# Kernel tuning notes

Hardware: AMD Instinct MI355X
Metric: run time of the kernel (lower is better)

The kernel has to match this reference:

```python
import jax, jax.numpy as jnp
import numpy as np

B, S, D, H = 32, 512, 768, 12
HD = D // H
FF = 4 * D
EPS = 1e-5


def layernorm(x, g, b):
    mu = jnp.mean(x, axis=-1, keepdims=True)
    var = jnp.mean(jnp.square(x - mu), axis=-1, keepdims=True)
    return (x - mu) * jax.lax.rsqrt(var + EPS) * g + b


def setup_inputs() -> dict:
    key = jax.random.key(0)
    ks = jax.random.split(key, 10)
    s = 0.02
    return {
        "x": jax.random.normal(ks[0], (B, S, D), jnp.float32),
        "edge_bias": jax.random.normal(ks[1], (H, S, S), jnp.float32) * s,
        "ln1_g": jnp.ones((D,), jnp.float32),
        "ln1_b": jnp.zeros((D,), jnp.float32),
        "qkv_w": jax.random.normal(ks[2], (3 * D, D), jnp.float32) * s,
        "qkv_b": jnp.zeros((3 * D,), jnp.float32),
        "proj_w": jax.random.normal(ks[3], (D, D), jnp.float32) * s,
        "proj_b": jnp.zeros((D,), jnp.float32),
        "ln2_g": jnp.ones((D,), jnp.float32),
        "ln2_b": jnp.zeros((D,), jnp.float32),
        "fc1_w": jax.random.normal(ks[4], (FF, D), jnp.float32) * s,
        "fc1_b": jnp.zeros((FF,), jnp.float32),
        "fc2_w": jax.random.normal(ks[5], (D, FF), jnp.float32) * s,
        "fc2_b": jnp.zeros((D,), jnp.float32),
    }


def reference(x, edge_bias, ln1_g, ln1_b, qkv_w, qkv_b, proj_w, proj_b,
              ln2_g, ln2_b, fc1_w, fc1_b, fc2_w, fc2_b):
    shortcut = x
    xn = layernorm(x, ln1_g, ln1_b)
    # qkv: [B,S,3D] -> [3,B,H,S,HD]
    qkv = (xn @ qkv_w.T + qkv_b).reshape(B, S, 3, H, HD).transpose(2, 0, 3, 1, 4)
    q, k, v = qkv[0], qkv[1], qkv[2]
    q = q * (HD ** -0.5)
    attn = jnp.einsum('bhqd,bhkd->bhqk', q, k) + edge_bias[None]
    attn = jax.nn.softmax(attn, axis=-1)
    o = jnp.einsum('bhqk,bhkd->bhqd', attn, v)
    o = o.transpose(0, 2, 1, 3).reshape(B, S, D)
    o = o @ proj_w.T + proj_b
    x = shortcut + o
    h = layernorm(x, ln2_g, ln2_b)
    h = jax.nn.gelu(h @ fc1_w.T + fc1_b, approximate=False)
    h = h @ fc2_w.T + fc2_b
    return x + h
```

## Files before the change

kernel.cpp:

```cpp
#include <hip/hip_runtime.h>

typedef unsigned short u16;
typedef unsigned int u32;
typedef float f32x4 __attribute__((ext_vector_type(4)));
typedef __bf16 bf16x8 __attribute__((ext_vector_type(8)));

__device__ __forceinline__ u16 f2bf(float f) {
  u32 u = __float_as_uint(f);
  u += 0x7fffu + ((u >> 16) & 1u);
  return (u16)(u >> 16);
}

__device__ __forceinline__ float bf2f(u16 v) {
  return __uint_as_float((u32)v << 16);
}

__device__ __forceinline__ void gload16(const u16* g, u16* l) {
  __builtin_amdgcn_global_load_lds(
      (__attribute__((address_space(1))) void*)(u16*)g,
      (__attribute__((address_space(3))) void*)l, 16, 0, 0);
}

__global__ __launch_bounds__(256) void cvt_bf16(const float* __restrict__ in,
                                                u16* __restrict__ o, int n4) {
  int i = blockIdx.x * 256 + threadIdx.x;
  if (i >= n4) return;
  float4 f = reinterpret_cast<const float4*>(in)[i];
  u32 lo = (u32)f2bf(f.x) | ((u32)f2bf(f.y) << 16);
  u32 hi = (u32)f2bf(f.z) | ((u32)f2bf(f.w) << 16);
  reinterpret_cast<uint2*>(o)[i] = make_uint2(lo, hi);
}

__global__ __launch_bounds__(256) void cvt_w_pack(const float* __restrict__ in,
                                                  u16* __restrict__ o, int N, int K) {
  int i = blockIdx.x * 256 + threadIdx.x;
  const int ng = K >> 3;
  if (i >= N * ng) return;
  const int n = i / ng;
  const int k = (i - n * ng) * 8;
  const float4 f0 = reinterpret_cast<const float4*>(in + (size_t)n * K + k)[0];
  const float4 f1 = reinterpret_cast<const float4*>(in + (size_t)n * K + k)[1];
  u32 p0 = (u32)f2bf(f0.x) | ((u32)f2bf(f0.y) << 16);
  u32 p1 = (u32)f2bf(f0.z) | ((u32)f2bf(f0.w) << 16);
  u32 p2 = (u32)f2bf(f1.x) | ((u32)f2bf(f1.y) << 16);
  u32 p3 = (u32)f2bf(f1.z) | ((u32)f2bf(f1.w) << 16);
  u16* dst = o + ((size_t)(k >> 5) * N + n) * 32 + (k & 31);
  reinterpret_cast<uint4*>(dst)[0] = make_uint4(p0, p1, p2, p3);
}

__global__ __launch_bounds__(256) void ln_bf16(const float* __restrict__ x,
                                               const float* __restrict__ g,
                                               const float* __restrict__ b,
                                               u16* __restrict__ o) {
  const int row = blockIdx.x;
  const int t = threadIdx.x;
  const float* xr = x + (size_t)row * 768;
  float a0 = xr[t], a1 = xr[t + 256], a2 = xr[t + 512];
  float s = a0 + a1 + a2;
  float ss = a0 * a0 + a1 * a1 + a2 * a2;
#pragma unroll
  for (int m = 1; m < 64; m <<= 1) {
    s += __shfl_xor(s, m);
    ss += __shfl_xor(ss, m);
  }
  __shared__ float sb[8];
  if ((t & 63) == 0) { sb[t >> 6] = s; sb[4 + (t >> 6)] = ss; }
  __syncthreads();
  s = sb[0] + sb[1] + sb[2] + sb[3];
  ss = sb[4] + sb[5] + sb[6] + sb[7];
  const float mu = s * (1.0f / 768.0f);
  const float var = ss * (1.0f / 768.0f) - mu * mu;
  const float rs = rsqrtf(var + 1e-5f);
#pragma unroll
  for (int c = 0; c < 3; ++c) {
    const int col = t + c * 256;
    const float a = (c == 0) ? a0 : (c == 1) ? a1 : a2;
    o[((size_t)(col >> 5) * 16384 + row) * 32 + (col & 31)] =
        f2bf((a - mu) * rs * g[col] + b[col]);
  }
}

enum { EPI_QKV = 0, EPI_PROJ = 1, EPI_GELU = 2, EPI_OUT = 3 };

template <int EPI>
__global__ __launch_bounds__(512, 2) void gemm_bt(
    const u16* __restrict__ A, const u16* __restrict__ W,
    const float* __restrict__ bias, const float* __restrict__ res,
    float* __restrict__ outf, u16* __restrict__ outb,
    u16* __restrict__ outq, u16* __restrict__ outk, u16* __restrict__ outv,
    int M, int N, int K) {
  __shared__ u16 SA[4 * 8192];
  __shared__ u16 SB[4 * 8192];
  const int tid = threadIdx.x;
  const int wid = tid >> 6, l = tid & 63;
  const int wm = wid >> 2, wn = wid & 3;
  const int lg = l >> 4, lc = l & 15;

  const u32 nbn = gridDim.x;
  const u32 orig = blockIdx.y * nbn + blockIdx.x;
  const u32 cpx = (nbn * gridDim.y) >> 3;
  const u32 wgid = (orig & 7) * cpx + (orig >> 3);
  const int bn = wgid % nbn;
  const int bm = wgid / nbn;

  const size_t Msl = (size_t)M * 32;
  const size_t Nsl = (size_t)N * 32;
  const size_t lane_a = (size_t)(bm * 256 + wid * 16 + (l >> 2)) * 32 +
                        (((l & 3) ^ ((l >> 3) & 3)) << 3);
  const size_t lane_w = (size_t)(bn * 256 + wid * 16 + (l >> 2)) * 32 +
                        (((l & 3) ^ ((l >> 3) & 3)) << 3);

  const int sg = (lg ^ ((lc >> 1) & 3)) << 3;

  f32x4 acc[8][4] = {};

  const int NU = K >> 5;

#define STAGE(u)                                                      \
  {                                                                   \
    const int slot_ = (u) & 3;                                        \
    const u16* Au_ = A + (size_t)(u) * Msl + lane_a;                  \
    const u16* Wu_ = W + (size_t)(u) * Nsl + lane_w;                  \
    gload16(Au_, &SA[slot_ * 8192 + wid * 512]);                      \
    gload16(Au_ + 4096, &SA[slot_ * 8192 + 4096 + wid * 512]);        \
    gload16(Wu_, &SB[slot_ * 8192 + wid * 512]);                      \
    gload16(Wu_ + 4096, &SB[slot_ * 8192 + 4096 + wid * 512]);        \
  }

  STAGE(0);
  STAGE(1);
  STAGE(2);
  asm volatile("s_waitcnt vmcnt(8)" ::: "memory");
  __builtin_amdgcn_s_barrier();

  for (int u = 0; u < NU; ++u) {
    const u16* sa = &SA[(u & 3) * 8192];
    const u16* sb = &SB[(u & 3) * 8192];
    bf16x8 af[8], bf[4];
#pragma unroll
    for (int mi = 0; mi < 8; ++mi)
      af[mi] = *reinterpret_cast<const bf16x8*>(&sa[(wm * 128 + mi * 16 + lc) * 32 + sg]);
#pragma unroll
    for (int ni = 0; ni < 4; ++ni)
      bf[ni] = *reinterpret_cast<const bf16x8*>(&sb[(wn * 64 + ni * 16 + lc) * 32 + sg]);
    if (u + 3 < NU) STAGE(u + 3);
    __builtin_amdgcn_s_barrier();
    __builtin_amdgcn_s_setprio(1);
#pragma unroll
    for (int mi = 0; mi < 8; ++mi)
#pragma unroll
      for (int ni = 0; ni < 4; ++ni)
        acc[mi][ni] = __builtin_amdgcn_mfma_f32_16x16x32_bf16(af[mi], bf[ni], acc[mi][ni], 0, 0, 0);
    __builtin_amdgcn_s_setprio(0);
    if (u + 3 < NU) {
      asm volatile("s_waitcnt vmcnt(8)" ::: "memory");
    } else if (u + 2 < NU) {
      asm volatile("s_waitcnt vmcnt(4)" ::: "memory");
    } else if (u + 1 < NU) {
      asm volatile("s_waitcnt vmcnt(0)" ::: "memory");
    }
    __builtin_amdgcn_s_barrier();
  }
#undef STAGE

  const int rbase = bm * 256 + wm * 128;
  const int cbase = bn * 256 + wn * 64;
#pragma unroll
  for (int mi = 0; mi < 8; ++mi) {
#pragma unroll
    for (int ni = 0; ni < 4; ++ni) {
#pragma unroll
      for (int r = 0; r < 4; ++r) {
        const int i = rbase + mi * 16 + lg * 4 + r;
        const int j = cbase + ni * 16 + lc;
        float v = acc[mi][ni][r] + bias[j];
        if constexpr (EPI == EPI_QKV) {
          const int t = j / 768;
          const int rr = j - t * 768;
          const int h = rr >> 6, hd = rr & 63;
          const int bb = i >> 9, ssi = i & 511;
          if (t == 0) {
            outq[((size_t)(bb * 12 + h) * 512 + ssi) * 64 + hd] = f2bf(v * 0.125f);
          } else if (t == 1) {
            outk[((size_t)(bb * 12 + h) * 512 + ssi) * 64 + hd] = f2bf(v);
          } else {
            outv[((size_t)(bb * 12 + h) * 64 + hd) * 512 + ssi] = f2bf(v);
          }
        } else if constexpr (EPI == EPI_PROJ) {
          outf[(size_t)i * 768 + j] = v + res[(size_t)i * 768 + j];
        } else if constexpr (EPI == EPI_GELU) {
          float gl = 0.5f * v * (1.0f + erff(v * 0.70710678118654752f));
          outb[((size_t)(j >> 5) * 16384 + i) * 32 + (j & 31)] = f2bf(gl);
        } else {
          outf[(size_t)i * 768 + j] = v + res[(size_t)i * 768 + j];
        }
      }
    }
  }
}

__global__ __launch_bounds__(256) void attn_fwd(const u16* __restrict__ q,
                                                const u16* __restrict__ k,
                                                const u16* __restrict__ vt,
                                                const u16* __restrict__ ebb,
                                                u16* __restrict__ o) {
  __shared__ u16 Ks[128 * 64];
  __shared__ u16 Vs[64 * 128];
  __shared__ u16 Bs[64 * 128];
  __shared__ u16 P[4 * 1024];
  const int tid = threadIdx.x;
  const int w = tid >> 6, l = tid & 63;
  const int lg = l >> 4, lc = l & 15;
  const int xcd = blockIdx.x & 7;
  const int wg = xcd * 384 + (blockIdx.x >> 3);
  const int qt = wg & 7;
  const int b = (wg >> 3) & 31;
  const int h = wg >> 8;
  const int bh = b * 12 + h;
  const int q0 = qt * 64;
  const u16* qp = q + (size_t)bh * 512 * 64;
  const u16* kp = k + (size_t)bh * 512 * 64;
  const u16* vtp = vt + (size_t)bh * 64 * 512;
  const u16* ep = ebb + (size_t)h * 262144 + (size_t)q0 * 512;

  bf16x8 aq[2];
#pragma unroll
  for (int kk = 0; kk < 2; ++kk)
    aq[kk] = *reinterpret_cast<const bf16x8*>(qp + (q0 + w * 16 + lc) * 64 + kk * 32 + lg * 8);

  float m[4], lsum[4];
  f32x4 oa[4] = {};
#pragma unroll
  for (int r = 0; r < 4; ++r) { m[r] = -1e30f; lsum[r] = 0.f; }

  const int krow_l = l >> 3;
  const int kgr = ((l & 7) ^ (l >> 3)) << 3;
  const int vrow_l = l >> 4;
  const int vswz = 4 * (w & 1) + (l >> 4);
  const int vgr = (((l & 15) ^ vswz)) << 3;
  const int bgr = (l & 15) << 3;
  char* Pw = (char*)&P[w * 1024];

  for (int kc = 0; kc < 4; ++kc) {
    const int kb = kc * 128;
    __syncthreads();
#pragma unroll
    for (int i = 0; i < 4; ++i) {
      const int grp = i * 4 + w;
      gload16(kp + (size_t)(kb + grp * 8 + krow_l) * 64 + kgr, &Ks[grp * 512]);
      gload16(vtp + (size_t)(grp * 4 + vrow_l) * 512 + kb + vgr, &Vs[grp * 512]);
      gload16(ep + (size_t)(grp * 4 + vrow_l) * 512 + kb + bgr, &Bs[grp * 512]);
    }
    __syncthreads();

    f32x4 s[8] = {};
#pragma unroll
    for (int kt = 0; kt < 8; ++kt) {
      const int kbyte = (kt * 16 + lc) * 128;
      const int sw = lc & 7;
      bf16x8 b0 = *reinterpret_cast<const bf16x8*>((const char*)Ks + kbyte + ((lg ^ sw) << 4));
      bf16x8 b1 = *reinterpret_cast<const bf16x8*>((const char*)Ks + kbyte + (((4 + lg) ^ sw) << 4));
      s[kt] = __builtin_amdgcn_mfma_f32_16x16x32_bf16(aq[0], b0, s[kt], 0, 0, 0);
      s[kt] = __builtin_amdgcn_mfma_f32_16x16x32_bf16(aq[1], b1, s[kt], 0, 0, 0);
    }
#pragma unroll
    for (int kt = 0; kt < 8; ++kt)
#pragma unroll
      for (int r = 0; r < 4; ++r)
        s[kt][r] += bf2f(Bs[(w * 16 + lg * 4 + r) * 128 + kt * 16 + lc]);
#pragma unroll
    for (int r = 0; r < 4; ++r) {
      float mc = s[0][r];
#pragma unroll
      for (int kt = 1; kt < 8; ++kt) mc = fmaxf(mc, s[kt][r]);
      mc = fmaxf(mc, __shfl_xor(mc, 1));
      mc = fmaxf(mc, __shfl_xor(mc, 2));
      mc = fmaxf(mc, __shfl_xor(mc, 4));
      mc = fmaxf(mc, __shfl_xor(mc, 8));
      const float mn = fmaxf(m[r], mc);
      const float al = __expf(m[r] - mn);
      m[r] = mn;
      float sum = 0.f;
#pragma unroll
      for (int kt = 0; kt < 8; ++kt) {
        float pv = __expf(s[kt][r] - mn);
        s[kt][r] = pv;
        sum += pv;
      }
      sum += __shfl_xor(sum, 1);
      sum += __shfl_xor(sum, 2);
      sum += __shfl_xor(sum, 4);
      sum += __shfl_xor(sum, 8);
      lsum[r] = lsum[r] * al + sum;
#pragma unroll
      for (int ni = 0; ni < 4; ++ni) oa[ni][r] *= al;
    }
#pragma unroll
    for (int kt = 0; kt < 8; ++kt)
#pragma unroll
      for (int r = 0; r < 4; ++r) {
        const int row = lg * 4 + r;
        int byte = (row << 8) + ((kt * 16 + lc) << 1);
        byte ^= (row & 7) << 4;
        *reinterpret_cast<u16*>(Pw + byte) = f2bf(s[kt][r]);
      }
#pragma unroll
    for (int ks = 0; ks < 4; ++ks) {
      int pbyte = (lc << 8) + ks * 64 + lg * 16;
      pbyte ^= (lc & 7) << 4;
      bf16x8 pa = *reinterpret_cast<const bf16x8*>(Pw + pbyte);
#pragma unroll
      for (int ni = 0; ni < 4; ++ni) {
        const int vbyte = (ni * 16 + lc) * 256 + (((ks * 4 + lg) ^ (lc & 7)) << 4);
        bf16x8 bv = *reinterpret_cast<const bf16x8*>((const char*)Vs + vbyte);
        oa[ni] = __builtin_amdgcn_mfma_f32_16x16x32_bf16(pa, bv, oa[ni], 0, 0, 0);
      }
    }
  }

  float inv[4];
#pragma unroll
  for (int r = 0; r < 4; ++r) inv[r] = 1.0f / lsum[r];
#pragma unroll
  for (int ni = 0; ni < 4; ++ni)
#pragma unroll
    for (int r = 0; r < 4; ++r) {
      const int i = b * 512 + q0 + w * 16 + lg * 4 + r;
      const int j = h * 64 + ni * 16 + lc;
      o[((size_t)(j >> 5) * 16384 + i) * 32 + (j & 31)] = f2bf(oa[ni][r] * inv[r]);
    }
}

extern "C" void kernel_launch(void* const* d_in, const int* in_sizes, int n_in,
                              void* d_out, int out_size, void* d_ws, size_t ws_size,
                              hipStream_t stream) {
  const float* x     = (const float*)d_in[0];
  const float* ebias = (const float*)d_in[1];
  const float* ln1g  = (const float*)d_in[2];
  const float* ln1b  = (const float*)d_in[3];
  const float* qkvw  = (const float*)d_in[4];
  const float* qkvb  = (const float*)d_in[5];
  const float* projw = (const float*)d_in[6];
  const float* projb = (const float*)d_in[7];
  const float* ln2g  = (const float*)d_in[8];
  const float* ln2b  = (const float*)d_in[9];
  const float* fc1w  = (const float*)d_in[10];
  const float* fc1b  = (const float*)d_in[11];
  const float* fc2w  = (const float*)d_in[12];
  const float* fc2b  = (const float*)d_in[13];
  float* out = (float*)d_out;

  char* p = (char*)d_ws;
  const size_t ACT = (size_t)16384 * 768 * 2;
  u16* xnb = (u16*)(p);
  u16* qb  = (u16*)(p + ACT);
  u16* kb  = (u16*)(p + 2 * ACT);
  u16* vb  = (u16*)(p + 3 * ACT);
  u16* ffb = (u16*)(p + 4 * ACT);
  u16* ebb = (u16*)(p + 4 * ACT);
  float* x2 = (float*)(p + 4 * ACT + (size_t)16384 * 3072 * 2);
  char* wz = p + 4 * ACT + (size_t)16384 * 3072 * 2 + (size_t)16384 * 768 * 4;
  u16* wq  = (u16*)wz;
  u16* wp  = wq + (size_t)2304 * 768;
  u16* wf1 = wp + (size_t)768 * 768;
  u16* wf2 = wf1 + (size_t)3072 * 768;

  cvt_w_pack<<<864, 256, 0, stream>>>(qkvw, wq, 2304, 768);
  cvt_w_pack<<<288, 256, 0, stream>>>(projw, wp, 768, 768);
  cvt_w_pack<<<1152, 256, 0, stream>>>(fc1w, wf1, 3072, 768);
  cvt_w_pack<<<1152, 256, 0, stream>>>(fc2w, wf2, 768, 3072);
  cvt_bf16<<<3072, 256, 0, stream>>>(ebias, ebb, 786432);

  ln_bf16<<<16384, 256, 0, stream>>>(x, ln1g, ln1b, xnb);

  gemm_bt<EPI_QKV><<<dim3(9, 64), 512, 0, stream>>>(
      xnb, wq, qkvb, nullptr, nullptr, nullptr, qb, kb, vb, 16384, 2304, 768);

  attn_fwd<<<3072, 256, 0, stream>>>(qb, kb, vb, ebb, xnb);

  gemm_bt<EPI_PROJ><<<dim3(3, 64), 512, 0, stream>>>(
      xnb, wp, projb, x, x2, nullptr, nullptr, nullptr, nullptr, 16384, 768, 768);

  ln_bf16<<<16384, 256, 0, stream>>>(x2, ln2g, ln2b, kb);

  gemm_bt<EPI_GELU><<<dim3(12, 64), 512, 0, stream>>>(
      kb, wf1, fc1b, nullptr, nullptr, ffb, nullptr, nullptr, nullptr, 16384, 3072, 768);

  gemm_bt<EPI_OUT><<<dim3(3, 64), 512, 0, stream>>>(
      ffb, wf2, fc2b, x2, out, nullptr, nullptr, nullptr, nullptr, 16384, 768, 3072);
}
```

Baseline: 536.9 us.

## Double-buffer GEMM register fragments across unrolled K steps; use tanh-form GELU

Unrolls the GEMM main loop by two and keeps two sets of register fragments, so LDS reads for the next K-slice are issued before the current MFMA block. The aim is to hide LDS latency behind matrix math and issue one wait/barrier pair per K-step. It also swaps the exact erf GELU for a sigmoid-form tanh approximation using fast exp and reciprocal, which cuts epilogue cost but departs slightly from exact GELU. The loop assumes an even number of K-slices and uses higher register pressure.

```diff
diff --git a/kernel.cpp b/kernel.cpp
--- a/kernel.cpp
+++ b/kernel.cpp
@@ -82,6 +82,27 @@
 
 enum { EPI_QKV = 0, EPI_PROJ = 1, EPI_GELU = 2, EPI_OUT = 3 };
 
+__device__ __forceinline__ void read_b4(const u16* sb_, int wn, int lc, int sg,
+                                        bf16x8* bf) {
+#pragma unroll
+  for (int ni = 0; ni < 4; ++ni)
+    bf[ni] = *reinterpret_cast<const bf16x8*>(&sb_[(wn * 64 + ni * 16 + lc) * 32 + sg]);
+}
+
+__device__ __forceinline__ void read_a01(const u16* sa_, int wm, int lc, int sg,
+                                         bf16x8* af) {
+#pragma unroll
+  for (int mi = 0; mi < 2; ++mi)
+    af[mi] = *reinterpret_cast<const bf16x8*>(&sa_[(wm * 128 + mi * 16 + lc) * 32 + sg]);
+}
+
+__device__ __forceinline__ void read_a27(const u16* sa_, int wm, int lc, int sg,
+                                         bf16x8* af) {
+#pragma unroll
+  for (int mi = 2; mi < 8; ++mi)
+    af[mi] = *reinterpret_cast<const bf16x8*>(&sa_[(wm * 128 + mi * 16 + lc) * 32 + sg]);
+}
+
 template <int EPI>
 __global__ __launch_bounds__(512, 2) void gemm_bt(
     const u16* __restrict__ A, const u16* __restrict__ W,
@@ -109,7 +130,6 @@
                         (((l & 3) ^ ((l >> 3) & 3)) << 3);
   const size_t lane_w = (size_t)(bn * 256 + wid * 16 + (l >> 2)) * 32 +
                         (((l & 3) ^ ((l >> 3) & 3)) << 3);
-
   const int sg = (lg ^ ((lc >> 1) & 3)) << 3;
 
   f32x4 acc[8][4] = {};
@@ -118,50 +138,62 @@
 
 #define STAGE(u)                                                      \
   {                                                                   \
-    const int slot_ = (u) & 3;                                        \
     const u16* Au_ = A + (size_t)(u) * Msl + lane_a;                  \
     const u16* Wu_ = W + (size_t)(u) * Nsl + lane_w;                  \
-    gload16(Au_, &SA[slot_ * 8192 + wid * 512]);                      \
-    gload16(Au_ + 4096, &SA[slot_ * 8192 + 4096 + wid * 512]);        \
-    gload16(Wu_, &SB[slot_ * 8192 + wid * 512]);                      \
-    gload16(Wu_ + 4096, &SB[slot_ * 8192 + 4096 + wid * 512]);        \
-  }
+    gload16(Au_, &SA[((u) & 3) * 8192 + wid * 512]);                  \
+    gload16(Au_ + 4096, &SA[((u) & 3) * 8192 + 4096 + wid * 512]);    \
+    gload16(Wu_, &SB[((u) & 3) * 8192 + wid * 512]);                  \
+    gload16(Wu_ + 4096, &SB[((u) & 3) * 8192 + 4096 + wid * 512]);    \
+  }
+
+#define MFMA32(AF, BF)                                                        \
+  {                                                                           \
+    __builtin_amdgcn_s_setprio(1);                                            \
+    _Pragma("unroll") for (int mi = 0; mi < 8; ++mi)                          \
+        _Pragma("unroll") for (int ni = 0; ni < 4; ++ni) acc[mi][ni] =        \
+            __builtin_amdgcn_mfma_f32_16x16x32_bf16(AF[mi], BF[ni],           \
+                                                    acc[mi][ni], 0, 0, 0);    \
+    __builtin_amdgcn_s_setprio(0);                                            \
+  }
+
+  bf16x8 afA[8], bfA[4], afB[8], bfB[4];
 
   STAGE(0);
   STAGE(1);
   STAGE(2);
-  asm volatile("s_waitcnt vmcnt(8)" ::: "memory");
+  asm volatile("s_waitcnt vmcnt(4)" ::: "memory");
   __builtin_amdgcn_s_barrier();
-
-  for (int u = 0; u < NU; ++u) {
-    const u16* sa = &SA[(u & 3) * 8192];
-    const u16* sb = &SB[(u & 3) * 8192];
-    bf16x8 af[8], bf[4];
-#pragma unroll
-    for (int mi = 0; mi < 8; ++mi)
-      af[mi] = *reinterpret_cast<const bf16x8*>(&sa[(wm * 128 + mi * 16 + lc) * 32 + sg]);
-#pragma unroll
-    for (int ni = 0; ni < 4; ++ni)
-      bf[ni] = *reinterpret_cast<const bf16x8*>(&sb[(wn * 64 + ni * 16 + lc) * 32 + sg]);
+  read_b4(&SB[0], wn, lc, sg, bfA);
+  read_a01(&SA[0], wm, lc, sg, afA);
+
+  for (int u = 0; u < NU; u += 2) {
+    read_a27(&SA[(u & 3) * 8192], wm, lc, sg, afA);
     if (u + 3 < NU) STAGE(u + 3);
+    read_b4(&SB[((u + 1) & 3) * 8192], wn, lc, sg, bfB);
+    read_a01(&SA[((u + 1) & 3) * 8192], wm, lc, sg, afB);
+    MFMA32(afA, bfA);
+    if (u + 3 < NU) {
+      asm volatile("s_waitcnt vmcnt(4)" ::: "memory");
+    } else if (u + 2 < NU) {
+      asm volatile("s_waitcnt vmcnt(0)" ::: "memory");
+    }
     __builtin_amdgcn_s_barrier();
-    __builtin_amdgcn_s_setprio(1);
-#pragma unroll
-    for (int mi = 0; mi < 8; ++mi)
-#pragma unroll
-      for (int ni = 0; ni < 4; ++ni)
-        acc[mi][ni] = __builtin_amdgcn_mfma_f32_16x16x32_bf16(af[mi], bf[ni], acc[mi][ni], 0, 0, 0);
-    __builtin_amdgcn_s_setprio(0);
-    if (u + 3 < NU) {
-      asm volatile("s_waitcnt vmcnt(8)" ::: "memory");
-    } else if (u + 2 < NU) {
+    read_a27(&SA[((u + 1) & 3) * 8192], wm, lc, sg, afB);
+    if (u + 4 < NU) STAGE(u + 4);
+    if (u + 2 < NU) {
+      read_b4(&SB[((u + 2) & 3) * 8192], wn, lc, sg, bfA);
+      read_a01(&SA[((u + 2) & 3) * 8192], wm, lc, sg, afA);
+    }
+    MFMA32(afB, bfB);
+    if (u + 4 < NU) {
       asm volatile("s_waitcnt vmcnt(4)" ::: "memory");
-    } else if (u + 1 < NU) {
+    } else if (u + 3 < NU) {
       asm volatile("s_waitcnt vmcnt(0)" ::: "memory");
     }
     __builtin_amdgcn_s_barrier();
   }
 #undef STAGE
+#undef MFMA32
 
   const int rbase = bm * 256 + wm * 128;
   const int cbase = bn * 256 + wn * 64;
@@ -189,7 +221,8 @@
         } else if constexpr (EPI == EPI_PROJ) {
           outf[(size_t)i * 768 + j] = v + res[(size_t)i * 768 + j];
         } else if constexpr (EPI == EPI_GELU) {
-          float gl = 0.5f * v * (1.0f + erff(v * 0.70710678118654752f));
+          float z = -1.5957691216f * v - 0.07135481627f * v * v * v;
+          float gl = v * __builtin_amdgcn_rcpf(1.0f + __expf(z));
           outb[((size_t)(j >> 5) * 16384 + i) * 32 + (j & 31)] = f2bf(gl);
         } else {
           outf[(size_t)i * 768 + j] = v + res[(size_t)i * 768 + j];
```

Result: no change. 533.2 us (-0.7%).
